# Performance work log

Hardware: AMD Instinct MI355X
Metric: run time of the kernel (lower is better)

The kernel has to match this reference:

```python
import jax, jax.numpy as jnp
import numpy as np

N = 2_000_000  # hits
D = 4          # track-parameter dim
P = 50_000     # number of particle ids (0 = noise)


def setup_inputs() -> dict:
    key = jax.random.key(0)
    k1, k2, k3, k4, k5 = jax.random.split(key, 5)
    # beta in (0, 1) open interval so arctanh stays finite
    beta = jax.random.uniform(k1, (N,), jnp.float32, 0.01, 0.99)
    pred = jax.random.normal(k2, (N, D), jnp.float32)
    track_params = jax.random.normal(k3, (N, D), jnp.float32)
    particle_id = jax.random.randint(k4, (N,), 0, P)
    reconstructable = jax.random.randint(k5, (N,), 0, 2)
    return {
        "beta": beta,
        "pred": pred,
        "particle_id": particle_id,
        "track_params": track_params,
        "reconstructable": reconstructable,
    }


def reference(beta, pred, particle_id, track_params, reconstructable):
    # mask = reconstructable > 0; instead of gathering a dynamic subset,
    # route masked-out hits (and pid==0 noise) to segment 0, which is dropped.
    valid = reconstructable > 0
    seg = jnp.where(valid, particle_id, 0)

    # per-hit squared-error summed over parameter dim (mse_loss reduction='none' then sum(dim=1))
    mse = jnp.sum((pred - track_params) ** 2, axis=1)  # [N]
    xi = jnp.arctanh(beta) ** 2                         # [N]

    # segmented replacement of the dense N x P pid_masks broadcast:
    # terms_p = sum_i mse_i * xi_i * [pid_i == p], xi_p_norm_p = sum_i xi_i * [pid_i == p]
    num = jax.ops.segment_sum(mse * xi, seg, num_segments=P)  # [P]
    den = jax.ops.segment_sum(xi, seg, num_segments=P)        # [P]

    # mean over real particle ids 1..P-1 (segment 0 holds noise + masked hits)
    return jnp.mean(num[1:] / den[1:])
```

## Files before the change

### kernel.cpp

```cpp
#include <hip/hip_runtime.h>

#define P_IDS   50000
#define NBUCK   32
#define BUCK_W  1563
#define HPT     8
#define BLK_HITS (256 * HPT)
#define M_PER   64
#define SUBB    16

struct Rec { int pid; float num; float den; };

__global__ void zero_out(float* __restrict__ out) {
    if (threadIdx.x == 0) *out = 0.0f;
}

__global__ void __launch_bounds__(256)
phaseA_bucket(const float* __restrict__ beta,
              const float4* __restrict__ pred,
              const int* __restrict__ pid_arr,
              const float4* __restrict__ track,
              const int* __restrict__ recon,
              int* __restrict__ cnt_arr,
              Rec* __restrict__ recs,
              int n, int nblk) {
    __shared__ int cursor[NBUCK];
    const int t = threadIdx.x;
    if (t < NBUCK) cursor[t] = 0;
    __syncthreads();

    const int B = blockIdx.x * BLK_HITS;

    #pragma unroll
    for (int h = 0; h < HPT; ++h) {
        int i = B + h * 256 + t;
        if (i < n) {
            int    p  = pid_arr[i];
            int    r  = recon[i];
            float  b  = beta[i];
            float4 pr = pred[i];
            float4 tp = track[i];
            float dx = pr.x - tp.x, dy = pr.y - tp.y;
            float dz = pr.z - tp.z, dw = pr.w - tp.w;
            float mse = dx*dx + dy*dy + dz*dz + dw*dw;
            float at = 0.5f * logf((1.0f + b) / (1.0f - b));
            float xi = at * at;
            if (r > 0 && p > 0) {
                int bb   = p / BUCK_W;
                int rank = atomicAdd(&cursor[bb], 1);
                if (rank < M_PER) {
                    Rec rr;
                    rr.pid = p;
                    rr.num = mse * xi;
                    rr.den = xi;
                    recs[((size_t)(bb * nblk + blockIdx.x)) * M_PER + rank] = rr;
                }
            }
        }
    }
    __syncthreads();
    if (t < NBUCK)
        cnt_arr[t * nblk + blockIdx.x] = min(cursor[t], M_PER);
}

__global__ void __launch_bounds__(256)
phaseB_bin(const int* __restrict__ cnt_arr,
           const Rec* __restrict__ recs,
           float2* __restrict__ partials,
           int nblk) {
    __shared__ float2 hist[BUCK_W];
    int part = blockIdx.x / SUBB;
    int sub  = blockIdx.x % SUBB;

    for (int j = threadIdx.x; j < BUCK_W; j += 256)
        hist[j] = make_float2(0.0f, 0.0f);
    __syncthreads();

    int lane  = threadIdx.x & 63;
    int wid   = threadIdx.x >> 6;
    int wslot = sub * 4 + wid;
    const int nslots = SUBB * 4;
    int pbase = part * BUCK_W;

    for (int b = wslot; b < nblk; b += nslots) {
        int cnt = cnt_arr[part * nblk + b];
        const Rec* r = recs + ((size_t)(part * nblk + b)) * M_PER;
        for (int idx = lane; idx < cnt; idx += 64) {
            Rec rr = r[idx];
            int local = rr.pid - pbase;
            atomicAdd(&hist[local].x, rr.num);
            atomicAdd(&hist[local].y, rr.den);
        }
    }
    __syncthreads();

    float2* dst = partials + (size_t)blockIdx.x * BUCK_W;
    for (int j = threadIdx.x; j < BUCK_W; j += 256)
        dst[j] = hist[j];
}

__global__ void __launch_bounds__(256)
phaseC_mean(const float2* __restrict__ partials,
            float* __restrict__ out) {
    double local = 0.0;
    int stride = gridDim.x * blockDim.x;
    for (int p = 1 + blockIdx.x * blockDim.x + threadIdx.x; p < P_IDS; p += stride) {
        int part = p / BUCK_W;
        int loc  = p % BUCK_W;
        const float2* base = partials + ((size_t)part * SUBB) * BUCK_W + loc;
        float num = 0.0f, den = 0.0f;
        #pragma unroll
        for (int s = 0; s < SUBB; ++s) {
            float2 v = base[(size_t)s * BUCK_W];
            num += v.x;
            den += v.y;
        }
        local += (double)(num / den);
    }

    for (int off = 32; off > 0; off >>= 1)
        local += __shfl_down(local, off, 64);

    __shared__ double wave_sums[4];
    int lane = threadIdx.x & 63;
    int wid  = threadIdx.x >> 6;
    if (lane == 0) wave_sums[wid] = local;
    __syncthreads();

    if (threadIdx.x == 0) {
        double s = wave_sums[0] + wave_sums[1] + wave_sums[2] + wave_sums[3];
        atomicAdd(out, (float)(s / (double)(P_IDS - 1)));
    }
}

__global__ void __launch_bounds__(256)
scatter_fallback(const float* __restrict__ beta,
                 const float4* __restrict__ pred,
                 const int* __restrict__ pid,
                 const float4* __restrict__ track,
                 const int* __restrict__ recon,
                 float2* __restrict__ bins, int n) {
    int i = blockIdx.x * blockDim.x + threadIdx.x;
    if (i >= n) return;
    int p = pid[i];
    int r = recon[i];
    if (r <= 0 || p <= 0) return;
    float  b  = beta[i];
    float4 pr = pred[i];
    float4 tp = track[i];
    float dx = pr.x - tp.x, dy = pr.y - tp.y, dz = pr.z - tp.z, dw = pr.w - tp.w;
    float mse = dx*dx + dy*dy + dz*dz + dw*dw;
    float at = 0.5f * logf((1.0f + b) / (1.0f - b));
    float xi = at * at;
    atomicAdd(&bins[p].x, mse * xi);
    atomicAdd(&bins[p].y, xi);
}

__global__ void __launch_bounds__(256)
reduce_fallback(const float2* __restrict__ bins, float* __restrict__ out) {
    double local = 0.0;
    int stride = gridDim.x * blockDim.x;
    for (int p = 1 + blockIdx.x * blockDim.x + threadIdx.x; p < P_IDS; p += stride) {
        float2 v = bins[p];
        local += (double)(v.x / v.y);
    }
    for (int off = 32; off > 0; off >>= 1)
        local += __shfl_down(local, off, 64);
    __shared__ double wave_sums[4];
    int lane = threadIdx.x & 63;
    int wid  = threadIdx.x >> 6;
    if (lane == 0) wave_sums[wid] = local;
    __syncthreads();
    if (threadIdx.x == 0) {
        double s = wave_sums[0] + wave_sums[1] + wave_sums[2] + wave_sums[3];
        atomicAdd(out, (float)(s / (double)(P_IDS - 1)));
    }
}

extern "C" void kernel_launch(void* const* d_in, const int* in_sizes, int n_in,
                              void* d_out, int out_size, void* d_ws, size_t ws_size,
                              hipStream_t stream) {
    const float*  beta  = (const float*)d_in[0];
    const float4* pred  = (const float4*)d_in[1];
    const int*    pid   = (const int*)d_in[2];
    const float4* track = (const float4*)d_in[3];
    const int*    recon = (const int*)d_in[4];
    float* out = (float*)d_out;
    int n = in_sizes[0];

    int nblk = (n + BLK_HITS - 1) / BLK_HITS;

    size_t recs_bytes = sizeof(Rec) * (size_t)NBUCK * nblk * M_PER;
    size_t recs_pad   = (recs_bytes + 255) & ~(size_t)255;
    size_t cnt_bytes  = sizeof(int) * (size_t)NBUCK * nblk;
    size_t cnt_pad    = (cnt_bytes + 255) & ~(size_t)255;
    size_t part_bytes = sizeof(float2) * (size_t)NBUCK * SUBB * BUCK_W;
    size_t needed = recs_pad + cnt_pad + part_bytes;

    if (ws_size >= needed) {
        Rec*    recs     = (Rec*)d_ws;
        int*    cnt_arr  = (int*)((char*)d_ws + recs_pad);
        float2* partials = (float2*)((char*)d_ws + recs_pad + cnt_pad);

        zero_out<<<1, 64, 0, stream>>>(out);

        phaseA_bucket<<<nblk, 256, 0, stream>>>(beta, pred, pid, track, recon,
                                                cnt_arr, recs, n, nblk);
        phaseB_bin<<<NBUCK * SUBB, 256, 0, stream>>>(cnt_arr, recs, partials, nblk);
        phaseC_mean<<<196, 256, 0, stream>>>(partials, out);
    } else {
        float2* bins = (float2*)d_ws;
        hipMemsetAsync(bins, 0, P_IDS * sizeof(float2), stream);
        hipMemsetAsync(d_out, 0, sizeof(float), stream);
        int grid = (n + 255) / 256;
        scatter_fallback<<<grid, 256, 0, stream>>>(beta, pred, pid, track, recon,
                                                   bins, n);
        reduce_fallback<<<196, 256, 0, stream>>>(bins, out);
    }
}
```

Baseline: 141.7 us.

## Pack bucket records into 8 bytes and stage them in LDS for coalesced writes

```diff
diff --git a/kernel.cpp b/kernel.cpp
--- a/kernel.cpp
+++ b/kernel.cpp
@@ -1,4 +1,5 @@
 #include <hip/hip_runtime.h>
+#include <stdint.h>
 
 #define P_IDS   50000
 #define NBUCK   32
@@ -8,7 +9,6 @@
 #define M_PER   64
 #define SUBB    16
 
-struct Rec { int pid; float num; float den; };
 
 __global__ void zero_out(float* __restrict__ out) {
     if (threadIdx.x == 0) *out = 0.0f;
@@ -21,8 +21,9 @@
               const float4* __restrict__ track,
               const int* __restrict__ recon,
               int* __restrict__ cnt_arr,
-              Rec* __restrict__ recs,
+              uint2* __restrict__ recs,
               int n, int nblk) {
+    __shared__ uint2 stage[NBUCK * M_PER];
     __shared__ int cursor[NBUCK];
     const int t = threadIdx.x;
     if (t < NBUCK) cursor[t] = 0;
@@ -45,26 +46,33 @@
             float at = 0.5f * logf((1.0f + b) / (1.0f - b));
             float xi = at * at;
             if (r > 0 && p > 0) {
-                int bb   = p / BUCK_W;
+                int bb = p / BUCK_W;
+                int pl = p - bb * BUCK_W;
                 int rank = atomicAdd(&cursor[bb], 1);
                 if (rank < M_PER) {
-                    Rec rr;
-                    rr.pid = p;
-                    rr.num = mse * xi;
-                    rr.den = xi;
-                    recs[((size_t)(bb * nblk + blockIdx.x)) * M_PER + rank] = rr;
+                    uint2 rr;
+                    rr.x = (__float_as_uint(xi) & 0xFFFFF800u) | (uint32_t)pl;
+                    rr.y = __float_as_uint(mse * xi);
+                    stage[bb * M_PER + rank] = rr;
                 }
             }
         }
     }
     __syncthreads();
+
+    const uint4* src = (const uint4*)stage;
+    uint4* dst = (uint4*)(recs + (size_t)blockIdx.x * (NBUCK * M_PER));
+    #pragma unroll
+    for (int k = 0; k < 4; ++k)
+        dst[t + k * 256] = src[t + k * 256];
+
     if (t < NBUCK)
-        cnt_arr[t * nblk + blockIdx.x] = min(cursor[t], M_PER);
+        cnt_arr[blockIdx.x * NBUCK + t] = min(cursor[t], M_PER);
 }
 
 __global__ void __launch_bounds__(256)
 phaseB_bin(const int* __restrict__ cnt_arr,
-           const Rec* __restrict__ recs,
+           const uint2* __restrict__ recs,
            float2* __restrict__ partials,
            int nblk) {
     __shared__ float2 hist[BUCK_W];
@@ -79,16 +87,17 @@
     int wid   = threadIdx.x >> 6;
     int wslot = sub * 4 + wid;
     const int nslots = SUBB * 4;
-    int pbase = part * BUCK_W;
 
     for (int b = wslot; b < nblk; b += nslots) {
-        int cnt = cnt_arr[part * nblk + b];
-        const Rec* r = recs + ((size_t)(part * nblk + b)) * M_PER;
+        int cnt = cnt_arr[b * NBUCK + part];
+        const uint2* r = recs + ((size_t)b * NBUCK + part) * M_PER;
         for (int idx = lane; idx < cnt; idx += 64) {
-            Rec rr = r[idx];
-            int local = rr.pid - pbase;
-            atomicAdd(&hist[local].x, rr.num);
-            atomicAdd(&hist[local].y, rr.den);
+            uint2 rr = r[idx];
+            int   pl  = rr.x & 0x7FFu;
+            float xi  = __uint_as_float(rr.x & 0xFFFFF800u);
+            float num = __uint_as_float(rr.y);
+            atomicAdd(&hist[pl].x, num);
+            atomicAdd(&hist[pl].y, xi);
         }
     }
     __syncthreads();
@@ -189,15 +198,15 @@
 
     int nblk = (n + BLK_HITS - 1) / BLK_HITS;
 
-    size_t recs_bytes = sizeof(Rec) * (size_t)NBUCK * nblk * M_PER;
+    size_t recs_bytes = sizeof(uint2) * (size_t)nblk * NBUCK * M_PER;
     size_t recs_pad   = (recs_bytes + 255) & ~(size_t)255;
-    size_t cnt_bytes  = sizeof(int) * (size_t)NBUCK * nblk;
+    size_t cnt_bytes  = sizeof(int) * (size_t)nblk * NBUCK;
     size_t cnt_pad    = (cnt_bytes + 255) & ~(size_t)255;
     size_t part_bytes = sizeof(float2) * (size_t)NBUCK * SUBB * BUCK_W;
     size_t needed = recs_pad + cnt_pad + part_bytes;
 
     if (ws_size >= needed) {
-        Rec*    recs     = (Rec*)d_ws;
+        uint2*  recs     = (uint2*)d_ws;
         int*    cnt_arr  = (int*)((char*)d_ws + recs_pad);
         float2* partials = (float2*)((char*)d_ws + recs_pad + cnt_pad);
 
```

Measured after the change: 136.5 us. 1.04x faster.
